# Kernel tuning notes

Hardware: AMD Instinct MI355X
Metric: run time of the kernel (lower is better)

The kernel has to match this reference:

```python
import jax, jax.numpy as jnp
import numpy as np

N_NODES = 100000
N_EDGES = 1600000
N_FEAT = 64
HIDDEN = 16


def setup_inputs() -> dict:
    key = jax.random.key(0)
    ks = jax.random.split(key, 10)
    x = jax.random.normal(ks[0], (N_NODES, N_FEAT), dtype=jnp.float32)
    edge_index = jax.random.randint(ks[1], (2, N_EDGES), 0, N_NODES, dtype=jnp.int64)
    As = jax.random.normal(ks[2], (2, N_EDGES), dtype=jnp.float32)
    ws_weights = jax.random.normal(ks[3], (2,), dtype=jnp.float32)
    Wl1 = jax.random.normal(ks[4], (N_FEAT, HIDDEN), dtype=jnp.float32) / np.sqrt(N_FEAT)
    bl1 = jnp.zeros((HIDDEN,), dtype=jnp.float32)
    Wr1 = jax.random.normal(ks[5], (N_FEAT, HIDDEN), dtype=jnp.float32) / np.sqrt(N_FEAT)
    Wl2 = jax.random.normal(ks[6], (HIDDEN, 1), dtype=jnp.float32) / np.sqrt(HIDDEN)
    bl2 = jnp.zeros((1,), dtype=jnp.float32)
    Wr2 = jax.random.normal(ks[7], (HIDDEN, 1), dtype=jnp.float32) / np.sqrt(HIDDEN)
    return {"x": x, "edge_index": edge_index, "As": As, "ws_weights": ws_weights,
            "Wl1": Wl1, "bl1": bl1, "Wr1": Wr1, "Wl2": Wl2, "bl2": bl2, "Wr2": Wr2}


def reference(x, edge_index, As, ws_weights, Wl1, bl1, Wr1, Wl2, bl2, Wr2):
    # WeightedSumLayer: weighted sum of per-edge weight vectors
    ewm = jnp.einsum('m,me->e', ws_weights, As)  # [E]
    # edge mask (nonzero weighted sum keeps the edge); instead of slicing to a
    # data-dependent edge count, zero out masked messages (same aggregation).
    mask = (ewm != 0).astype(x.dtype)  # [E]
    src, dst = edge_index[0], edge_index[1]
    n = x.shape[0]

    # SAGEConv layer 1 (aggr='sum'): out = lin_l(sum_j x_j) + lin_r(x)
    msg1 = x[src] * mask[:, None]                             # [E, F]
    agg1 = jax.ops.segment_sum(msg1, dst, num_segments=n)     # [N, F]
    h = jax.nn.relu(agg1 @ Wl1 + bl1 + x @ Wr1)               # [N, H]

    # SAGEConv layer 2
    msg2 = h[src] * mask[:, None]                             # [E, H]
    agg2 = jax.ops.segment_sum(msg2, dst, num_segments=n)     # [N, H]
    out = agg2 @ Wl2 + bl2 + h @ Wr2                          # [N, 1]
    return out
```

## Files before the change

kernel.cpp:

```cpp
#include <hip/hip_runtime.h>
#include <hip/hip_bf16.h>

constexpr int NN = 100000;
constexpr int NE = 1600000;
constexpr int NF = 64;
constexpr int NH = 16;

constexpr int NPB  = 128;
constexpr int LB   = 7;
constexpr int NBKT = (NN + NPB - 1) / NPB;
constexpr int CAP  = 2560;
constexpr int TB   = 512;
constexpr int CHUNK = 8192;
constexpr int NBF   = (NE + CHUNK - 1) / CHUNK;
constexpr int NBG   = (NN + 255) / 256;
constexpr int FD = NBKT + 1;

constexpr int SMEM_BYTES = CHUNK * 2 + NBKT * 4 + FD * 4 + 32;

__device__ __forceinline__ float bf16_to_f32(unsigned short u) {
    return __uint_as_float(((unsigned int)u) << 16);
}
__device__ __forceinline__ unsigned short f32_to_bf16(float f) {
    __hip_bfloat16 hb = __float2bfloat16(f);
    return *reinterpret_cast<unsigned short*>(&hb);
}

__global__ __launch_bounds__(TB)
void k_fused(const float* __restrict__ x,
             const float* __restrict__ Wl1,
             const float* __restrict__ Wr1,
             unsigned short* __restrict__ p,
             float* __restrict__ r,
             const int* __restrict__ ei, const float* __restrict__ As,
             const float* __restrict__ ws,
             unsigned int* __restrict__ gchunk, int* __restrict__ fdir)
{
    __shared__ __align__(16) char smem[SMEM_BYTES];
    int m3  = blockIdx.x % 3;
    int d3  = blockIdx.x / 3;
    int role = (m3 == 2);
    int rb   = role ? d3 : d3 * 2 + m3;
    int tid  = threadIdx.x;

    if (role == 0) {
        float* sW = (float*)smem;
        for (int i = tid; i < NF * NH; i += TB) {
            sW[i]           = Wl1[i];
            sW[NF * NH + i] = Wr1[i];
        }
        __syncthreads();

        int half = tid >> 8;
        int ln   = tid & 255;
        int n = rb * 256 + ln;
        if (n >= NN) return;

        const float* W = sW + half * (NF * NH);
        float acc[NH];
#pragma unroll
        for (int j = 0; j < NH; ++j) acc[j] = 0.f;

        const float4* xr = reinterpret_cast<const float4*>(x + (size_t)n * NF);
#pragma unroll
        for (int k4 = 0; k4 < NF / 4; ++k4) {
            float4 v = xr[k4];
            float xs[4] = {v.x, v.y, v.z, v.w};
#pragma unroll
            for (int t2 = 0; t2 < 4; ++t2) {
                const float* wrow = &W[(k4 * 4 + t2) * NH];
#pragma unroll
                for (int j = 0; j < NH; ++j)
                    acc[j] = fmaf(xs[t2], wrow[j], acc[j]);
            }
        }

        if (half == 0) {
            unsigned int pu[8];
#pragma unroll
            for (int j2 = 0; j2 < 8; ++j2)
                pu[j2] = (unsigned int)f32_to_bf16(acc[2*j2]) |
                         ((unsigned int)f32_to_bf16(acc[2*j2+1]) << 16);
            uint4* pp = reinterpret_cast<uint4*>(p + (size_t)n * NH);
            pp[0] = make_uint4(pu[0], pu[1], pu[2], pu[3]);
            pp[1] = make_uint4(pu[4], pu[5], pu[6], pu[7]);
        } else {
            float4* rp = reinterpret_cast<float4*>(r + (size_t)n * NH);
#pragma unroll
            for (int j4 = 0; j4 < NH / 4; ++j4)
                rp[j4] = make_float4(acc[j4*4], acc[j4*4+1], acc[j4*4+2], acc[j4*4+3]);
        }
    } else {
        unsigned short* srk  = (unsigned short*)smem;
        int* lcnt  = (int*)(smem + CHUNK * 2);
        int* fscan = lcnt + NBKT;
        int* wsum  = fscan + FD;

        for (int i = tid; i < NBKT; i += TB) lcnt[i] = 0;
        __syncthreads();

        int base = rb * CHUNK;
        float w0 = ws[0], w1 = ws[1];

#pragma unroll
        for (int j = 0; j < CHUNK / TB; ++j) {
            int idx = j * TB + tid;
            int e = base + idx;
            unsigned short rk = 0xFFFFu;
            if (e < NE) {
                float ewm = w0 * As[e] + w1 * As[NE + e];
                if (ewm != 0.f)
                    rk = (unsigned short)atomicAdd(&lcnt[ei[NE + e] >> LB], 1);
            }
            srk[idx] = rk;
        }
        __syncthreads();

        {
            int loc[2]; int s0 = 0;
#pragma unroll
            for (int g = 0; g < 2; ++g) {
                int idx = tid * 2 + g;
                int v = (idx < NBKT) ? lcnt[idx] : 0;
                loc[g] = s0; s0 += v;
            }
            int lane = tid & 63, w = tid >> 6;
            int si = s0;
#pragma unroll
            for (int off = 1; off < 64; off <<= 1) {
                int u = __shfl_up(si, off);
                if (lane >= off) si += u;
            }
            if (lane == 63) wsum[w] = si;
            __syncthreads();
            int bse = 0;
            for (int i = 0; i < w; ++i) bse += wsum[i];
            int excl = bse + si - s0;
#pragma unroll
            for (int g = 0; g < 2; ++g) {
                int idx = tid * 2 + g;
                if (idx < NBKT) fscan[idx] = excl + loc[g];
            }
            if (tid == TB - 1) fscan[NBKT] = bse + si;
        }
        __syncthreads();

        for (int i = tid; i < FD; i += TB)
            fdir[(size_t)rb * FD + i] = fscan[i];

#pragma unroll
        for (int j = 0; j < CHUNK / TB; ++j) {
            int idx = j * TB + tid;
            unsigned short rk = srk[idx];
            if (rk != 0xFFFFu) {
                int e   = base + idx;
                int dst = ei[NE + e];
                int bk  = dst >> LB;
                gchunk[(size_t)rb * CHUNK + fscan[bk] + rk] =
                    ((unsigned)ei[e] << LB) | (unsigned)(dst & (NPB - 1));
            }
        }
    }
}

__global__ __launch_bounds__(256)
void k_agg1(const int* __restrict__ fdir, const unsigned int* __restrict__ gchunk,
            unsigned int* __restrict__ bmem,
            const unsigned short* __restrict__ p, const float* __restrict__ r,
            const float* __restrict__ bl1, const float* __restrict__ Wl2,
            const float* __restrict__ bl2, const float* __restrict__ Wr2,
            float* __restrict__ q, float* __restrict__ out,
            int* __restrict__ gsoff)
{
    __shared__ unsigned int sbm[CAP];
    __shared__ unsigned int ssorted[CAP];
    __shared__ int fstart[NBF];
    __shared__ int foff[NBF + 1];
    __shared__ int tscan[256];
    __shared__ int hist[NPB];
    __shared__ int hscan[NPB];
    __shared__ int soff[NPB + 1];

    int b = blockIdx.x;
    int tid = threadIdx.x;
    if (tid < NPB) hist[tid] = 0;

    {
        int sz = 0;
        if (tid < NBF) {
            int s0 = fdir[(size_t)tid * FD + b];
            int s1 = fdir[(size_t)tid * FD + b + 1];
            fstart[tid] = s0;
            sz = s1 - s0;
        }
        tscan[tid] = sz;
        __syncthreads();
        for (int off = 1; off < 256; off <<= 1) {
            int u = (tid >= off) ? tscan[tid - off] : 0;
            __syncthreads();
            tscan[tid] += u;
            __syncthreads();
        }
        if (tid < NBF) foff[tid] = tscan[tid] - sz;
        if (tid == 255) foff[NBF] = tscan[255];
    }
    __syncthreads();

    int cnt = min(foff[NBF], CAP);

    {
        int grp = tid >> 4, k = tid & 15;
        for (int f = grp; f < NBF; f += 16) {
            int o  = foff[f];
            int sz = foff[f + 1] - o;
            int s  = fstart[f];
            const unsigned int* src = gchunk + (size_t)f * CHUNK + s;
            int lim = min(sz, CAP - o);
            for (int j = k; j < lim; j += 16)
                sbm[o + j] = src[j];
        }
    }
    __syncthreads();

    int rk[CAP / 256];
#pragma unroll
    for (int j = 0; j < CAP / 256; ++j) {
        int i = j * 256 + tid;
        if (i < cnt)
            rk[j] = atomicAdd(&hist[sbm[i] & (NPB - 1)], 1);
    }
    __syncthreads();

    if (tid < NPB) hscan[tid] = hist[tid];
    __syncthreads();
    for (int off = 1; off < NPB; off <<= 1) {
        int u = (tid < NPB && tid >= off) ? hscan[tid - off] : 0;
        __syncthreads();
        if (tid < NPB) hscan[tid] += u;
        __syncthreads();
    }
    if (tid < NPB) soff[tid + 1] = hscan[tid];
    if (tid == 0) soff[0] = 0;
    __syncthreads();

#pragma unroll
    for (int j = 0; j < CAP / 256; ++j) {
        int i = j * 256 + tid;
        if (i < cnt) {
            unsigned int w = sbm[i];
            ssorted[soff[w & (NPB - 1)] + rk[j]] = w;
        }
    }
    __syncthreads();

    for (int i = tid; i < cnt; i += 256)
        bmem[(size_t)b * CAP + i] = ssorted[i];
    if (tid < NPB + 1)
        gsoff[(size_t)b * (NPB + 1) + tid] = soff[tid];

    int g = tid >> 4, k = tid & 15;
    int n0 = b * NPB;
#pragma unroll
    for (int jj = 0; jj < 8; ++jj) {
        int nl = g * 8 + jj;
        int s = soff[nl], e = soff[nl + 1];
        float a = 0.f;
        int i = s;
        for (; i + 3 < e; i += 4) {
            unsigned w0 = ssorted[i], w1 = ssorted[i+1], w2 = ssorted[i+2], w3 = ssorted[i+3];
            float v0 = bf16_to_f32(p[(size_t)(w0 >> LB) * NH + k]);
            float v1 = bf16_to_f32(p[(size_t)(w1 >> LB) * NH + k]);
            float v2 = bf16_to_f32(p[(size_t)(w2 >> LB) * NH + k]);
            float v3 = bf16_to_f32(p[(size_t)(w3 >> LB) * NH + k]);
            a += (v0 + v1) + (v2 + v3);
        }
        for (; i < e; ++i)
            a += bf16_to_f32(p[(size_t)(ssorted[i] >> LB) * NH + k]);

        int n = n0 + nl;
        if (n < NN) {
            float h = a + r[(size_t)n * NH + k] + bl1[k];
            h = h > 0.f ? h : 0.f;
            float qv = h * Wl2[k];
            float sv = h * Wr2[k];
#pragma unroll
            for (int m = 8; m >= 1; m >>= 1) {
                qv += __shfl_xor(qv, m);
                sv += __shfl_xor(sv, m);
            }
            if (k == 0) {
                q[n]   = qv;
                out[n] = sv + bl2[0];
            }
        }
    }
}

__global__ __launch_bounds__(256)
void k_agg2(const int* __restrict__ gsoff, const unsigned int* __restrict__ bmem,
            const float* __restrict__ q, float* __restrict__ out)
{
    int t = blockIdx.x * 256 + threadIdx.x;
    int n = t >> 2;
    int sub = t & 3;
    if (n >= NN) return;
    int b  = n >> LB;
    int dl = n & (NPB - 1);
    int s = gsoff[(size_t)b * (NPB + 1) + dl];
    int e = gsoff[(size_t)b * (NPB + 1) + dl + 1];
    const unsigned int* bm = bmem + (size_t)b * CAP;

    float a = 0.f;
    for (int i = s + sub; i < e; i += 4)
        a += q[bm[i] >> LB];
    a += __shfl_xor(a, 1);
    a += __shfl_xor(a, 2);
    if (sub == 0) out[n] += a;
}

extern "C" void kernel_launch(void* const* d_in, const int* in_sizes, int n_in,
                              void* d_out, int out_size, void* d_ws, size_t ws_size,
                              hipStream_t stream)
{
    const float* x   = (const float*)d_in[0];
    const int*   ei  = (const int*)  d_in[1];
    const float* As  = (const float*)d_in[2];
    const float* ws  = (const float*)d_in[3];
    const float* Wl1 = (const float*)d_in[4];
    const float* bl1 = (const float*)d_in[5];
    const float* Wr1 = (const float*)d_in[6];
    const float* Wl2 = (const float*)d_in[7];
    const float* bl2 = (const float*)d_in[8];
    const float* Wr2 = (const float*)d_in[9];
    float* out = (float*)d_out;

    unsigned short* p      = (unsigned short*)d_ws;
    float*          r      = (float*)(p + (size_t)NN * NH);
    float*          q      = r + (size_t)NN * NH;
    int*            gsoff  = (int*)(q + NN);
    int*            fdir   = gsoff + (size_t)NBKT * (NPB + 1);
    unsigned int*   gchunk = (unsigned int*)(fdir + (size_t)NBF * FD);
    unsigned int*   bmem   = gchunk + (size_t)NBF * CHUNK;

    int nblk = 3 * NBF;
    k_fused<<<nblk, TB, 0, stream>>>(x, Wl1, Wr1, p, r, ei, As, ws, gchunk, fdir);
    k_agg1<<<NBKT, 256, 0, stream>>>(fdir, gchunk, bmem, p, r, bl1, Wl2, bl2, Wr2,
                                     q, out, gsoff);
    k_agg2<<<(NN * 4 + 255) / 256, 256, 0, stream>>>(gsoff, bmem, q, out);
}
```

Before: 174.6 us.

## Transpose bucket directory, use wave-shuffle scans, and widen fused blocks to 1024

The per-chunk bucket offset directory is now stored transposed, so the aggregation kernel reads it with coalesced loads instead of strided ones. The shared-memory Hillis-Steele scans in the aggregation kernel become wave-level shuffle scans with a small cross-wave fixup, which removes many barriers. The fused kernel moves to 1024-thread blocks. Each GEMM thread now computes both the lin_l and lin_r projections for one node, and each binning block scans one bucket per thread. This halves the number of blocks and doubles the accumulators per thread, which may lower occupancy and reduce latency hiding.

```diff
diff --git a/kernel.cpp b/kernel.cpp
--- a/kernel.cpp
+++ b/kernel.cpp
@@ -10,13 +10,13 @@
 constexpr int LB   = 7;
 constexpr int NBKT = (NN + NPB - 1) / NPB;
 constexpr int CAP  = 2560;
-constexpr int TB   = 512;
+constexpr int TB   = 1024;
 constexpr int CHUNK = 8192;
 constexpr int NBF   = (NE + CHUNK - 1) / CHUNK;
-constexpr int NBG   = (NN + 255) / 256;
+constexpr int NBG   = (NN + TB - 1) / TB;
 constexpr int FD = NBKT + 1;
 
-constexpr int SMEM_BYTES = CHUNK * 2 + NBKT * 4 + FD * 4 + 32;
+constexpr int SMEM_BYTES = CHUNK * 2 + NBKT * 4 + FD * 4 + 64;
 
 __device__ __forceinline__ float bf16_to_f32(unsigned short u) {
     return __uint_as_float(((unsigned int)u) << 16);
@@ -34,13 +34,13 @@
              float* __restrict__ r,
              const int* __restrict__ ei, const float* __restrict__ As,
              const float* __restrict__ ws,
-             unsigned int* __restrict__ gchunk, int* __restrict__ fdir)
+             unsigned int* __restrict__ gchunk, int* __restrict__ fdirT)
 {
     __shared__ __align__(16) char smem[SMEM_BYTES];
     int m3  = blockIdx.x % 3;
     int d3  = blockIdx.x / 3;
-    int role = (m3 == 2);
-    int rb   = role ? d3 : d3 * 2 + m3;
+    int role = (m3 != 0);
+    int rb   = role ? d3 * 2 + (m3 - 1) : d3;
     int tid  = threadIdx.x;
 
     if (role == 0) {
@@ -51,15 +51,12 @@
         }
         __syncthreads();
 
-        int half = tid >> 8;
-        int ln   = tid & 255;
-        int n = rb * 256 + ln;
+        int n = rb * TB + tid;
         if (n >= NN) return;
 
-        const float* W = sW + half * (NF * NH);
-        float acc[NH];
-#pragma unroll
-        for (int j = 0; j < NH; ++j) acc[j] = 0.f;
+        float aL[NH], aR[NH];
+#pragma unroll
+        for (int j = 0; j < NH; ++j) { aL[j] = 0.f; aR[j] = 0.f; }
 
         const float4* xr = reinterpret_cast<const float4*>(x + (size_t)n * NF);
 #pragma unroll
@@ -68,28 +65,29 @@
             float xs[4] = {v.x, v.y, v.z, v.w};
 #pragma unroll
             for (int t2 = 0; t2 < 4; ++t2) {
-                const float* wrow = &W[(k4 * 4 + t2) * NH];
-#pragma unroll
-                for (int j = 0; j < NH; ++j)
-                    acc[j] = fmaf(xs[t2], wrow[j], acc[j]);
-            }
-        }
-
-        if (half == 0) {
-            unsigned int pu[8];
-#pragma unroll
-            for (int j2 = 0; j2 < 8; ++j2)
-                pu[j2] = (unsigned int)f32_to_bf16(acc[2*j2]) |
-                         ((unsigned int)f32_to_bf16(acc[2*j2+1]) << 16);
-            uint4* pp = reinterpret_cast<uint4*>(p + (size_t)n * NH);
-            pp[0] = make_uint4(pu[0], pu[1], pu[2], pu[3]);
-            pp[1] = make_uint4(pu[4], pu[5], pu[6], pu[7]);
-        } else {
-            float4* rp = reinterpret_cast<float4*>(r + (size_t)n * NH);
-#pragma unroll
-            for (int j4 = 0; j4 < NH / 4; ++j4)
-                rp[j4] = make_float4(acc[j4*4], acc[j4*4+1], acc[j4*4+2], acc[j4*4+3]);
-        }
+                const float* wl = &sW[(k4 * 4 + t2) * NH];
+                const float* wr = &sW[NF * NH + (k4 * 4 + t2) * NH];
+#pragma unroll
+                for (int j = 0; j < NH; ++j) {
+                    aL[j] = fmaf(xs[t2], wl[j], aL[j]);
+                    aR[j] = fmaf(xs[t2], wr[j], aR[j]);
+                }
+            }
+        }
+
+        unsigned int pu[8];
+#pragma unroll
+        for (int j2 = 0; j2 < 8; ++j2)
+            pu[j2] = (unsigned int)f32_to_bf16(aL[2*j2]) |
+                     ((unsigned int)f32_to_bf16(aL[2*j2+1]) << 16);
+        uint4* pp = reinterpret_cast<uint4*>(p + (size_t)n * NH);
+        pp[0] = make_uint4(pu[0], pu[1], pu[2], pu[3]);
+        pp[1] = make_uint4(pu[4], pu[5], pu[6], pu[7]);
+
+        float4* rp = reinterpret_cast<float4*>(r + (size_t)n * NH);
+#pragma unroll
+        for (int j4 = 0; j4 < NH / 4; ++j4)
+            rp[j4] = make_float4(aR[j4*4], aR[j4*4+1], aR[j4*4+2], aR[j4*4+3]);
     } else {
         unsigned short* srk  = (unsigned short*)smem;
         int* lcnt  = (int*)(smem + CHUNK * 2);
@@ -117,15 +115,9 @@
         __syncthreads();
 
         {
-            int loc[2]; int s0 = 0;
-#pragma unroll
-            for (int g = 0; g < 2; ++g) {
-                int idx = tid * 2 + g;
-                int v = (idx < NBKT) ? lcnt[idx] : 0;
-                loc[g] = s0; s0 += v;
-            }
+            int v = (tid < NBKT) ? lcnt[tid] : 0;
             int lane = tid & 63, w = tid >> 6;
-            int si = s0;
+            int si = v;
 #pragma unroll
             for (int off = 1; off < 64; off <<= 1) {
                 int u = __shfl_up(si, off);
@@ -135,18 +127,13 @@
             __syncthreads();
             int bse = 0;
             for (int i = 0; i < w; ++i) bse += wsum[i];
-            int excl = bse + si - s0;
-#pragma unroll
-            for (int g = 0; g < 2; ++g) {
-                int idx = tid * 2 + g;
-                if (idx < NBKT) fscan[idx] = excl + loc[g];
-            }
+            if (tid < NBKT) fscan[tid] = bse + si - v;
             if (tid == TB - 1) fscan[NBKT] = bse + si;
         }
         __syncthreads();
 
         for (int i = tid; i < FD; i += TB)
-            fdir[(size_t)rb * FD + i] = fscan[i];
+            fdirT[(size_t)i * NBF + rb] = fscan[i];
 
 #pragma unroll
         for (int j = 0; j < CHUNK / TB; ++j) {
@@ -164,7 +151,7 @@
 }
 
 __global__ __launch_bounds__(256)
-void k_agg1(const int* __restrict__ fdir, const unsigned int* __restrict__ gchunk,
+void k_agg1(const int* __restrict__ fdirT, const unsigned int* __restrict__ gchunk,
             unsigned int* __restrict__ bmem,
             const unsigned short* __restrict__ p, const float* __restrict__ r,
             const float* __restrict__ bl1, const float* __restrict__ Wl2,
@@ -176,10 +163,9 @@
     __shared__ unsigned int ssorted[CAP];
     __shared__ int fstart[NBF];
     __shared__ int foff[NBF + 1];
-    __shared__ int tscan[256];
     __shared__ int hist[NPB];
-    __shared__ int hscan[NPB];
     __shared__ int soff[NPB + 1];
+    __shared__ int wsum4[4];
 
     int b = blockIdx.x;
     int tid = threadIdx.x;
@@ -188,21 +174,24 @@
     {
         int sz = 0;
         if (tid < NBF) {
-            int s0 = fdir[(size_t)tid * FD + b];
-            int s1 = fdir[(size_t)tid * FD + b + 1];
+            int s0 = fdirT[(size_t)b * NBF + tid];
+            int s1 = fdirT[(size_t)(b + 1) * NBF + tid];
             fstart[tid] = s0;
             sz = s1 - s0;
         }
-        tscan[tid] = sz;
-        __syncthreads();
-        for (int off = 1; off < 256; off <<= 1) {
-            int u = (tid >= off) ? tscan[tid - off] : 0;
-            __syncthreads();
-            tscan[tid] += u;
-            __syncthreads();
-        }
-        if (tid < NBF) foff[tid] = tscan[tid] - sz;
-        if (tid == 255) foff[NBF] = tscan[255];
+        int lane = tid & 63, w = tid >> 6;
+        int si = sz;
+#pragma unroll
+        for (int off = 1; off < 64; off <<= 1) {
+            int u = __shfl_up(si, off);
+            if (lane >= off) si += u;
+        }
+        if (lane == 63) wsum4[w] = si;
+        __syncthreads();
+        int bse = 0;
+        for (int i = 0; i < w; ++i) bse += wsum4[i];
+        if (tid < NBF) foff[tid] = bse + si - sz;
+        if (tid == 255) foff[NBF] = bse + si;
     }
     __syncthreads();
 
@@ -231,16 +220,22 @@
     }
     __syncthreads();
 
-    if (tid < NPB) hscan[tid] = hist[tid];
-    __syncthreads();
-    for (int off = 1; off < NPB; off <<= 1) {
-        int u = (tid < NPB && tid >= off) ? hscan[tid - off] : 0;
-        __syncthreads();
-        if (tid < NPB) hscan[tid] += u;
-        __syncthreads();
-    }
-    if (tid < NPB) soff[tid + 1] = hscan[tid];
-    if (tid == 0) soff[0] = 0;
+    {
+        int v = (tid < NPB) ? hist[tid] : 0;
+        int lane = tid & 63, w = tid >> 6;
+        int si = v;
+#pragma unroll
+        for (int off = 1; off < 64; off <<= 1) {
+            int u = __shfl_up(si, off);
+            if (lane >= off) si += u;
+        }
+        if (lane == 63) wsum4[w] = si;
+        __syncthreads();
+        int bse = 0;
+        for (int i = 0; i < w; ++i) bse += wsum4[i];
+        if (tid < NPB) soff[tid + 1] = bse + si;
+        if (tid == 0) soff[0] = 0;
+    }
     __syncthreads();
 
 #pragma unroll
@@ -338,13 +333,13 @@
     float*          r      = (float*)(p + (size_t)NN * NH);
     float*          q      = r + (size_t)NN * NH;
     int*            gsoff  = (int*)(q + NN);
-    int*            fdir   = gsoff + (size_t)NBKT * (NPB + 1);
-    unsigned int*   gchunk = (unsigned int*)(fdir + (size_t)NBF * FD);
+    int*            fdirT  = gsoff + (size_t)NBKT * (NPB + 1);
+    unsigned int*   gchunk = (unsigned int*)(fdirT + (size_t)FD * NBF);
     unsigned int*   bmem   = gchunk + (size_t)NBF * CHUNK;
 
-    int nblk = 3 * NBF;
-    k_fused<<<nblk, TB, 0, stream>>>(x, Wl1, Wr1, p, r, ei, As, ws, gchunk, fdir);
-    k_agg1<<<NBKT, 256, 0, stream>>>(fdir, gchunk, bmem, p, r, bl1, Wl2, bl2, Wr2,
+    int nblk = 3 * NBG;
+    k_fused<<<nblk, TB, 0, stream>>>(x, Wl1, Wr1, p, r, ei, As, ws, gchunk, fdirT);
+    k_agg1<<<NBKT, 256, 0, stream>>>(fdirT, gchunk, bmem, p, r, bl1, Wl2, bl2, Wr2,
                                      q, out, gsoff);
     k_agg2<<<(NN * 4 + 255) / 256, 256, 0, stream>>>(gsoff, bmem, q, out);
 }
```

Result: slower. 182.6 us (+4.5%).
